# Performance work log

Measured on AMD Instinct MI355X. Metric: run time of the kernel, lower is better.

The kernel has to match this reference:

```python
import jax, jax.numpy as jnp
import numpy as np

B, N, M = 16, 2048, 2048


def setup_inputs() -> dict:
    key = jax.random.key(0)
    k1, k2, k3 = jax.random.split(key, 3)
    pred_dsmat = jax.random.uniform(k1, (B, N, M), dtype=jnp.float32)
    # valid sizes: src_ns <= tgt_ns so a permutation GT exists for every valid row
    src_ns = jax.random.randint(k2, (B,), 1024, 1537, dtype=jnp.int32)
    tgt_ns = jax.random.randint(k3, (B,), 1537, 2049, dtype=jnp.int32)
    # gt_perm: identity permutation restricted to the valid region (one 1 per valid row)
    i = jnp.arange(N)[:, None]
    j = jnp.arange(M)[None, :]
    eye = (i == j).astype(jnp.float32)  # [N, M]
    row_mask = (jnp.arange(N)[None, :] < src_ns[:, None]).astype(jnp.float32)  # [B, N]
    gt_perm = eye[None, :, :] * row_mask[:, :, None]  # [B, N, M]
    return {"pred_dsmat": pred_dsmat, "gt_perm": gt_perm,
            "src_ns": src_ns, "tgt_ns": tgt_ns, "beta_value": 0.1}


def reference(pred_dsmat, gt_perm, src_ns, tgt_ns, beta_value):
    Bn, Nn, Mn = pred_dsmat.shape
    row_mask = jnp.arange(Nn)[None, :] < src_ns[:, None]   # [B, N] bool
    col_mask = jnp.arange(Mn)[None, :] < tgt_ns[:, None]   # [B, M] bool
    mask = row_mask[:, :, None] & col_mask[:, None, :]     # [B, N, M]

    pred = jnp.clip(pred_dsmat, 0.0, 1.0) * mask
    gt = gt_perm * mask

    gt_pred = pred * gt                      # gt-selected predicted values
    row_gt = gt_pred.sum(axis=2)             # [B, N] per-row GT value
    col_gt = gt_pred.sum(axis=1)             # [B, M] per-col GT value
    row_cnt = gt.sum(axis=2)                 # [B, N] #GT matches per row
    col_cnt = gt.sum(axis=1)                 # [B, M] #GT matches per col

    # attention masks: entries >= (gt value - beta), restricted to valid region
    att_src = ((pred >= row_gt[:, :, None] - beta_value) & mask) * row_cnt[:, :, None]
    att_tgt = ((pred >= col_gt[:, None, :] - beta_value) & mask) * col_cnt[:, None, :]

    src_neg = jnp.sum(((att_src - gt) * pred) ** 2, axis=2)  # [B, N]
    src_pos = jnp.sum(gt_pred ** 2, axis=2)                  # [B, N]
    tgt_neg = jnp.sum(((att_tgt - gt) * pred) ** 2, axis=1)  # [B, M]

    # sum of tgt_neg over the GT-matched column of each row == dot with column counts
    corr = jnp.einsum('bm,bm->b', tgt_neg, col_cnt)          # [B]

    denom = 1.0 + src_neg + corr[:, None]                    # [B, N]
    num = jnp.where(row_mask, src_pos, 1.0)
    den = jnp.where(row_mask, denom, 1.0)
    loss = -0.5 * jnp.sum(jnp.log(num / den) * row_mask)
    n_sum = src_ns.sum().astype(pred.dtype)
    return loss / n_sum
```

## Files before the change

### kernel.cpp

```cpp
#include <hip/hip_runtime.h>

#define B_ 16
#define N_ 2048
#define M_ 2048
#define RROWS 8
#define WROWS 2
#define CHUNK 1024
#define NCHUNK (M_ / CHUNK)
#define JCH (CHUNK / 256)
#define DROWS 32
#define DWROWS 8
#define KCAP 4

__device__ __forceinline__ float wave_sum(float v) {
#pragma unroll
    for (int off = 32; off >= 1; off >>= 1) v += __shfl_xor(v, off);
    return v;
}

extern "C" __global__ __launch_bounds__(256) void k_gt(
    const float* __restrict__ gt, const float* __restrict__ pred,
    const int* __restrict__ src_ns, const int* __restrict__ tgt_ns,
    int* __restrict__ nnz, int* __restrict__ ent_col,
    float* __restrict__ ent_val,
    float* __restrict__ row_gt, float* __restrict__ row_cnt,
    float* __restrict__ colS_gt, float* __restrict__ colS_cnt,
    int* flag)
{
    const int b = blockIdx.y;
    const int src = src_ns[b];
    const int band = blockIdx.x;
    if (band * RROWS >= src) return;
    const int tgt = tgt_ns[b];
    const int c0 = blockIdx.z * CHUNK;
    if (tgt - c0 <= 0) return;
    const int wave = threadIdx.x >> 6, lane = threadIdx.x & 63;
    const int bfull = b * (N_ * M_);
    const int bc = bfull + c0;

    const int row0 = band * RROWS + wave * WROWS;
    for (int r = 0; r < WROWS; ++r) {
        const int n = row0 + r;
        if (n >= src) break;
        const int ri = b * N_ + n;
        const float4* grow = (const float4*)(gt + bc + n * M_);
        const float4 g0 = grow[lane];
        const float4 g1 = grow[64 + lane];
        const float4 g2 = grow[128 + lane];
        const float4 g3 = grow[192 + lane];
#define GTEST(GV, J) \
        if (GV.x != 0.f || GV.y != 0.f || GV.z != 0.f || GV.w != 0.f) { \
            const int mb = c0 + (J * 64 + lane) * 4; \
            GC(GV, 0, x); GC(GV, 1, y); GC(GV, 2, z); GC(GV, 3, w); \
        }
#define GC(GV, KK, MB) do { \
    const int c = mb + KK; \
    const float gv = GV.MB; \
    if (gv != 0.f && c < tgt) { \
        const int slot = atomicAdd(&nnz[ri], 1); \
        if (slot < KCAP) { \
            ent_col[ri * KCAP + slot] = c; ent_val[ri * KCAP + slot] = gv; \
            float pv = pred[bfull + n * M_ + c]; \
            pv = fminf(fmaxf(pv, 0.f), 1.f); \
            const float gp = gv * pv; \
            atomicAdd(&row_gt[ri], gp); \
            atomicAdd(&row_cnt[ri], gv); \
            atomicAdd(&colS_gt[b * M_ + c], gp); \
            atomicAdd(&colS_cnt[b * M_ + c], gv); \
        } else *flag = 1; \
    } \
} while (0)
        GTEST(g0, 0) GTEST(g1, 1) GTEST(g2, 2) GTEST(g3, 3)
#undef GC
#undef GTEST
    }
}

extern "C" __global__ __launch_bounds__(256) void k_p1d(
    const float* __restrict__ pred, const float* __restrict__ gt,
    const int* __restrict__ src_ns, const int* __restrict__ tgt_ns,
    const int* flag,
    float* __restrict__ row_gt, float* __restrict__ row_cnt,
    float* __restrict__ colD_gt, float* __restrict__ colD_cnt)
{
    if (*flag == 0) return;
    const int b = blockIdx.y;
    const int src = src_ns[b];
    const int band = blockIdx.x;
    if (band * DROWS >= src) return;
    const int tgt = tgt_ns[b];
    const int wave = threadIdx.x >> 6, lane = threadIdx.x & 63;
    const int base = b * (N_ * M_);

    float4 acg[8], accn[8];
#pragma unroll
    for (int j = 0; j < 8; ++j) { acg[j] = make_float4(0,0,0,0); accn[j] = make_float4(0,0,0,0); }

    const int row0 = band * DROWS + wave * DWROWS;
    for (int r = 0; r < DWROWS; ++r) {
        const int n = row0 + r;
        if (n >= src) break;
        const float4* prow = (const float4*)(pred + base + n * M_);
        const float4* grow = (const float4*)(gt + base + n * M_);
        float rg = 0.f, rc = 0.f;
#pragma unroll
        for (int j = 0; j < 8; ++j) {
            const int m4 = j * 64 + lane;
            const float4 p4 = prow[m4];
            const float4 g4 = grow[m4];
            const int mb = m4 * 4;
#define P1C(KK, MB) do { \
    const bool ok = (mb + KK) < tgt; \
    float p = fminf(fmaxf(p4.MB, 0.f), 1.f); p = ok ? p : 0.f; \
    const float g = ok ? g4.MB : 0.f; \
    const float gp = p * g; \
    rg += gp; rc += g; \
    acg[j].MB += gp; accn[j].MB += g; \
} while (0)
            P1C(0, x); P1C(1, y); P1C(2, z); P1C(3, w);
#undef P1C
        }
        rg = wave_sum(rg); rc = wave_sum(rc);
        if (lane == 0) { row_gt[b * N_ + n] = rg; row_cnt[b * N_ + n] = rc; }
    }

    __shared__ float4 s_cg[M_ / 4];
    __shared__ float4 s_cc[M_ / 4];
    for (int i = threadIdx.x; i < M_ / 4; i += 256) {
        s_cg[i] = make_float4(0,0,0,0);
        s_cc[i] = make_float4(0,0,0,0);
    }
    __syncthreads();
    for (int w = 0; w < 4; ++w) {
        if (wave == w) {
#pragma unroll
            for (int j = 0; j < 8; ++j) {
                const int i = j * 64 + lane;
                float4 v = s_cg[i];
                v.x += acg[j].x; v.y += acg[j].y; v.z += acg[j].z; v.w += acg[j].w;
                s_cg[i] = v;
                float4 u = s_cc[i];
                u.x += accn[j].x; u.y += accn[j].y; u.z += accn[j].z; u.w += accn[j].w;
                s_cc[i] = u;
            }
        }
        __syncthreads();
    }
    const float* fcg = (const float*)s_cg;
    const float* fcc = (const float*)s_cc;
    for (int i = threadIdx.x; i < M_; i += 256) {
        atomicAdd(&colD_gt[b * M_ + i], fcg[i]);
        atomicAdd(&colD_cnt[b * M_ + i], fcc[i]);
    }
}

extern "C" __global__ __launch_bounds__(256) void k_pred(
    const float* __restrict__ pred, const float* __restrict__ gt,
    const int* __restrict__ src_ns, const int* __restrict__ tgt_ns,
    const float* __restrict__ beta_p,
    const float* __restrict__ row_gt, const float* __restrict__ row_cnt,
    const float* __restrict__ colS_gt, const float* __restrict__ colS_cnt,
    const float* __restrict__ colD_gt, const float* __restrict__ colD_cnt,
    const int* __restrict__ nnz, const int* __restrict__ ent_col,
    const float* __restrict__ ent_val, const int* flag,
    float* __restrict__ src_neg, float* __restrict__ src_pos,
    float* __restrict__ corr)
{
    const int b = blockIdx.y;
    const int src = src_ns[b];
    const int band = blockIdx.x;
    if (band * RROWS >= src) return;
    const int tgt = tgt_ns[b];
    const int c0 = blockIdx.z * CHUNK;
    const bool chunk0 = (c0 == 0);
    if (tgt - c0 <= 0 && !chunk0) return;
    const float beta = beta_p[0];
    const int wave = threadIdx.x >> 6, lane = threadIdx.x & 63;
    const int bfull = b * (N_ * M_);
    const int bc = bfull + c0;
    const bool dense = (*flag != 0);
    const float* __restrict__ cgq = dense ? colD_gt : colS_gt;
    const float* __restrict__ ccq = dense ? colD_cnt : colS_cnt;

    float4 cgb[JCH], cc[JCH], tn[JCH];
    const float4* cg4 = (const float4*)(cgq + b * M_ + c0);
    const float4* cc4 = (const float4*)(ccq + b * M_ + c0);
#pragma unroll
    for (int j = 0; j < JCH; ++j) {
        float4 v = cg4[j * 64 + lane];
        v.x -= beta; v.y -= beta; v.z -= beta; v.w -= beta;
        cgb[j] = v;
        cc[j] = cc4[j * 64 + lane];
        tn[j] = make_float4(0,0,0,0);
    }

    float cadd = 0.f;
    const int row0 = band * RROWS + wave * WROWS;
    if (!dense) {
        for (int r = 0; r < WROWS; ++r) {
            const int n = row0 + r;
            if (n >= src) break;
            const int ri = b * N_ + n;
            const float rc = row_cnt[ri];
            const float rth = row_gt[ri] - beta;
            const float4* prow = (const float4*)(pred + bc + n * M_);
            const float4 p0 = prow[lane];
            const float4 p1 = prow[64 + lane];
            const float4 p2 = prow[128 + lane];
            const float4 p3 = prow[192 + lane];
            float sneg = 0.f;
#define P2S(PV, J, KK, MB) do { \
    const bool ok = (c0 + (J * 64 + lane) * 4 + KK) < tgt; \
    float p = fminf(fmaxf(PV.MB, 0.f), 1.f); p = ok ? p : 0.f; \
    const float as = (p >= rth) ? rc : 0.f; \
    const float ds = as * p; \
    sneg += ds * ds; \
    const float at = (p >= cgb[J].MB) ? cc[J].MB : 0.f; \
    const float d = at * p; \
    tn[J].MB += d * d; \
} while (0)
#define P2SV(PV, J) P2S(PV, J, 0, x); P2S(PV, J, 1, y); P2S(PV, J, 2, z); P2S(PV, J, 3, w);
            P2SV(p0, 0) P2SV(p1, 1) P2SV(p2, 2) P2SV(p3, 3)
#undef P2SV
#undef P2S
            sneg = wave_sum(sneg);
            if (lane == 0) {
                if (chunk0) {
                    float spos = 0.f;
                    const int nn0 = nnz[ri];
                    const int nn = nn0 < KCAP ? nn0 : KCAP;
                    for (int s = 0; s < nn; ++s) {
                        const int c = ent_col[ri * KCAP + s];
                        const float gv = ent_val[ri * KCAP + s];
                        float pv = pred[bfull + n * M_ + c];
                        pv = fminf(fmaxf(pv, 0.f), 1.f);
                        const float as = (pv >= rth) ? rc : 0.f;
                        const float d0 = as * pv;
                        const float d1 = (as - gv) * pv;
                        sneg += d1 * d1 - d0 * d0;
                        const float gp = gv * pv;
                        spos += gp * gp;
                        const float ccv = ccq[b * M_ + c];
                        const float at = (pv >= cgq[b * M_ + c] - beta) ? ccv : 0.f;
                        const float t0 = at * pv;
                        const float t1 = (at - gv) * pv;
                        cadd += (t1 * t1 - t0 * t0) * ccv;
                    }
                    atomicAdd(&src_pos[ri], spos);
                }
                atomicAdd(&src_neg[ri], sneg);
            }
        }
    } else {
        for (int r = 0; r < WROWS; ++r) {
            const int n = row0 + r;
            if (n >= src) break;
            const int ri = b * N_ + n;
            const float rc = row_cnt[ri];
            const float rth = row_gt[ri] - beta;
            const float4* prow = (const float4*)(pred + bc + n * M_);
            const float4* grow = (const float4*)(gt + bc + n * M_);
            const float4 p0 = prow[lane];
            const float4 p1 = prow[64 + lane];
            const float4 p2 = prow[128 + lane];
            const float4 p3 = prow[192 + lane];
            const float4 g0 = grow[lane];
            const float4 g1 = grow[64 + lane];
            const float4 g2 = grow[128 + lane];
            const float4 g3 = grow[192 + lane];
            float sneg = 0.f, spos = 0.f;
#define P2D(PV, GV, J, KK, MB) do { \
    const bool ok = (c0 + (J * 64 + lane) * 4 + KK) < tgt; \
    float p = fminf(fmaxf(PV.MB, 0.f), 1.f); p = ok ? p : 0.f; \
    const float gv = ok ? GV.MB : 0.f; \
    const float as = (p >= rth) ? rc : 0.f; \
    const float ds = (as - gv) * p; \
    sneg += ds * ds; \
    const float gp = gv * p; spos += gp * gp; \
    const float at = (p >= cgb[J].MB) ? cc[J].MB : 0.f; \
    const float dt = (at - gv) * p; \
    tn[J].MB += dt * dt; \
} while (0)
#define P2DV(PV, GV, J) P2D(PV, GV, J, 0, x); P2D(PV, GV, J, 1, y); P2D(PV, GV, J, 2, z); P2D(PV, GV, J, 3, w);
            P2DV(p0, g0, 0) P2DV(p1, g1, 1) P2DV(p2, g2, 2) P2DV(p3, g3, 3)
#undef P2DV
#undef P2D
            sneg = wave_sum(sneg); spos = wave_sum(spos);
            if (lane == 0) {
                atomicAdd(&src_neg[ri], sneg);
                atomicAdd(&src_pos[ri], spos);
            }
        }
    }

    float dp = cadd;
#pragma unroll
    for (int j = 0; j < JCH; ++j)
        dp += tn[j].x * cc[j].x + tn[j].y * cc[j].y + tn[j].z * cc[j].z + tn[j].w * cc[j].w;
    dp = wave_sum(dp);
    __shared__ float sred[4];
    if (lane == 0) sred[wave] = dp;
    __syncthreads();
    if (threadIdx.x == 0)
        atomicAdd(&corr[b], sred[0] + sred[1] + sred[2] + sred[3]);
}

extern "C" __global__ __launch_bounds__(256) void k_final(
    const float* __restrict__ src_neg, const float* __restrict__ src_pos,
    const float* __restrict__ corr_p, const int* __restrict__ src_ns,
    float* __restrict__ out)
{
    const int b = blockIdx.x >> 3;
    const int part = blockIdx.x & 7;
    const int wave = threadIdx.x >> 6, lane = threadIdx.x & 63;
    const int src = src_ns[b];
    const int n0 = part * (N_ / 8);
    const float corr = corr_p[b];

    float ls = 0.f;
    const int n = n0 + threadIdx.x;
    if (n < src) {
        const float sp = src_pos[b * N_ + n];
        const float sn = src_neg[b * N_ + n];
        ls = logf(sp) - logf(1.f + sn + corr);
    }
    ls = wave_sum(ls);
    __shared__ float sredl[4];
    if (lane == 0) sredl[wave] = ls;
    __syncthreads();
    if (threadIdx.x == 0) {
        const float total = sredl[0] + sredl[1] + sredl[2] + sredl[3];
        if (total != 0.f) {
            float nsum = 0.f;
            for (int i = 0; i < B_; ++i) nsum += (float)src_ns[i];
            atomicAdd(out, -0.5f * total / nsum);
        }
    }
}

extern "C" void kernel_launch(void* const* d_in, const int* in_sizes, int n_in,
                              void* d_out, int out_size, void* d_ws, size_t ws_size,
                              hipStream_t stream)
{
    const float* pred   = (const float*)d_in[0];
    const float* gtp    = (const float*)d_in[1];
    const int*   src_ns = (const int*)d_in[2];
    const int*   tgt_ns = (const int*)d_in[3];
    const float* beta   = (const float*)d_in[4];
    float* out = (float*)d_out;
    float* ws  = (float*)d_ws;

    float* colS_gt  = ws;
    float* colS_cnt = colS_gt  + B_ * M_;
    float* colD_gt  = colS_cnt + B_ * M_;
    float* colD_cnt = colD_gt  + B_ * M_;
    float* row_gt   = colD_cnt + B_ * M_;
    float* row_cnt  = row_gt   + B_ * N_;
    float* src_neg  = row_cnt  + B_ * N_;
    float* src_pos  = src_neg  + B_ * N_;
    float* corr     = src_pos  + B_ * N_;
    int*   nnz      = (int*)(corr + B_);
    int*   flag     = nnz + B_ * N_;
    int*   ent_col  = (int*)(flag + 1);
    float* ent_val  = (float*)(ent_col + B_ * N_ * KCAP);

    const size_t zero_bytes = (size_t)(4 * B_ * M_ + 5 * B_ * N_ + B_ + 1) * sizeof(float);
    hipMemsetAsync(d_ws, 0, zero_bytes, stream);
    hipMemsetAsync(d_out, 0, sizeof(float), stream);

    dim3 gsplit(N_ / RROWS, B_, NCHUNK);
    k_gt<<<gsplit, 256, 0, stream>>>(gtp, pred, src_ns, tgt_ns,
                                     nnz, ent_col, ent_val,
                                     row_gt, row_cnt, colS_gt, colS_cnt, flag);
    k_p1d<<<dim3(N_ / DROWS, B_), 256, 0, stream>>>(pred, gtp, src_ns, tgt_ns, flag,
                                                    row_gt, row_cnt, colD_gt, colD_cnt);
    k_pred<<<gsplit, 256, 0, stream>>>(pred, gtp, src_ns, tgt_ns, beta,
                                       row_gt, row_cnt,
                                       colS_gt, colS_cnt, colD_gt, colD_cnt,
                                       nnz, ent_col, ent_val, flag,
                                       src_neg, src_pos, corr);
    k_final<<<B_ * 8, 256, 0, stream>>>(src_neg, src_pos, corr, src_ns, out);
}
```

Baseline: 515.9 us.

## Prefetch next row in gt and sparse loss kernels, double rows per wave, precompute column masks

Doubles the rows handled per block and per wave (RROWS 16, WROWS 4). The k_gt scan and the sparse path of the loss kernel now software-pipeline their row loads, issuing the next row's float4 loads before processing the current row. The per-element column bound check is replaced by float masks computed once per chunk and applied by multiplication. Together these aim to hide memory latency and cut per-element ALU work, at the cost of more registers and half as many blocks.

```diff
diff --git a/kernel.cpp b/kernel.cpp
--- a/kernel.cpp
+++ b/kernel.cpp
@@ -3,8 +3,8 @@
 #define B_ 16
 #define N_ 2048
 #define M_ 2048
-#define RROWS 8
-#define WROWS 2
+#define RROWS 16
+#define WROWS 4
 #define CHUNK 1024
 #define NCHUNK (M_ / CHUNK)
 #define JCH (CHUNK / 256)
@@ -39,15 +39,26 @@
     const int bc = bfull + c0;
 
     const int row0 = band * RROWS + wave * WROWS;
-    for (int r = 0; r < WROWS; ++r) {
+    int rmax = src - row0; if (rmax > WROWS) rmax = WROWS;
+    if (rmax <= 0) return;
+
+    const float* gbase = gt + bc + row0 * M_;
+    const float4* grow = (const float4*)gbase;
+    float4 a0 = grow[lane];
+    float4 a1 = grow[64 + lane];
+    float4 a2 = grow[128 + lane];
+    float4 a3 = grow[192 + lane];
+    for (int r = 0; r < rmax; ++r) {
+        float4 b0, b1, b2, b3;
+        if (r + 1 < rmax) {
+            const float4* nrow = (const float4*)(gbase + (r + 1) * M_);
+            b0 = nrow[lane]; b1 = nrow[64 + lane];
+            b2 = nrow[128 + lane]; b3 = nrow[192 + lane];
+        } else {
+            b0 = b1 = b2 = b3 = make_float4(0,0,0,0);
+        }
         const int n = row0 + r;
-        if (n >= src) break;
         const int ri = b * N_ + n;
-        const float4* grow = (const float4*)(gt + bc + n * M_);
-        const float4 g0 = grow[lane];
-        const float4 g1 = grow[64 + lane];
-        const float4 g2 = grow[128 + lane];
-        const float4 g3 = grow[192 + lane];
 #define GTEST(GV, J) \
         if (GV.x != 0.f || GV.y != 0.f || GV.z != 0.f || GV.w != 0.f) { \
             const int mb = c0 + (J * 64 + lane) * 4; \
@@ -70,9 +81,10 @@
         } else *flag = 1; \
     } \
 } while (0)
-        GTEST(g0, 0) GTEST(g1, 1) GTEST(g2, 2) GTEST(g3, 3)
+        GTEST(a0, 0) GTEST(a1, 1) GTEST(a2, 2) GTEST(a3, 3)
 #undef GC
 #undef GTEST
+        a0 = b0; a1 = b1; a2 = b2; a3 = b3;
     }
 }
 
@@ -182,7 +194,7 @@
     const float* __restrict__ cgq = dense ? colD_gt : colS_gt;
     const float* __restrict__ ccq = dense ? colD_cnt : colS_cnt;
 
-    float4 cgb[JCH], cc[JCH], tn[JCH];
+    float4 cgb[JCH], cc[JCH], tn[JCH], msk[JCH];
     const float4* cg4 = (const float4*)(cgq + b * M_ + c0);
     const float4* cc4 = (const float4*)(ccq + b * M_ + c0);
 #pragma unroll
@@ -192,26 +204,41 @@
         cgb[j] = v;
         cc[j] = cc4[j * 64 + lane];
         tn[j] = make_float4(0,0,0,0);
+        const int mb = c0 + (j * 64 + lane) * 4;
+        msk[j].x = (mb + 0 < tgt) ? 1.f : 0.f;
+        msk[j].y = (mb + 1 < tgt) ? 1.f : 0.f;
+        msk[j].z = (mb + 2 < tgt) ? 1.f : 0.f;
+        msk[j].w = (mb + 3 < tgt) ? 1.f : 0.f;
     }
 
     float cadd = 0.f;
     const int row0 = band * RROWS + wave * WROWS;
+    int rmax = src - row0; if (rmax > WROWS) rmax = WROWS;
+
     if (!dense) {
-        for (int r = 0; r < WROWS; ++r) {
-            const int n = row0 + r;
-            if (n >= src) break;
-            const int ri = b * N_ + n;
-            const float rc = row_cnt[ri];
-            const float rth = row_gt[ri] - beta;
-            const float4* prow = (const float4*)(pred + bc + n * M_);
-            const float4 p0 = prow[lane];
-            const float4 p1 = prow[64 + lane];
-            const float4 p2 = prow[128 + lane];
-            const float4 p3 = prow[192 + lane];
-            float sneg = 0.f;
-#define P2S(PV, J, KK, MB) do { \
-    const bool ok = (c0 + (J * 64 + lane) * 4 + KK) < tgt; \
-    float p = fminf(fmaxf(PV.MB, 0.f), 1.f); p = ok ? p : 0.f; \
+        if (rmax > 0) {
+            const float* pbase = pred + bc + row0 * M_;
+            const float4* prow = (const float4*)pbase;
+            float4 a0 = prow[lane];
+            float4 a1 = prow[64 + lane];
+            float4 a2 = prow[128 + lane];
+            float4 a3 = prow[192 + lane];
+            for (int r = 0; r < rmax; ++r) {
+                float4 q0, q1, q2, q3;
+                if (r + 1 < rmax) {
+                    const float4* nrow = (const float4*)(pbase + (r + 1) * M_);
+                    q0 = nrow[lane]; q1 = nrow[64 + lane];
+                    q2 = nrow[128 + lane]; q3 = nrow[192 + lane];
+                } else {
+                    q0 = q1 = q2 = q3 = make_float4(0,0,0,0);
+                }
+                const int n = row0 + r;
+                const int ri = b * N_ + n;
+                const float rc = row_cnt[ri];
+                const float rth = row_gt[ri] - beta;
+                float sneg = 0.f;
+#define P2S(PV, J, MB) do { \
+    const float p = fminf(fmaxf(PV.MB, 0.f), 1.f) * msk[J].MB; \
     const float as = (p >= rth) ? rc : 0.f; \
     const float ds = as * p; \
     sneg += ds * ds; \
@@ -219,42 +246,43 @@
     const float d = at * p; \
     tn[J].MB += d * d; \
 } while (0)
-#define P2SV(PV, J) P2S(PV, J, 0, x); P2S(PV, J, 1, y); P2S(PV, J, 2, z); P2S(PV, J, 3, w);
-            P2SV(p0, 0) P2SV(p1, 1) P2SV(p2, 2) P2SV(p3, 3)
+#define P2SV(PV, J) P2S(PV, J, x); P2S(PV, J, y); P2S(PV, J, z); P2S(PV, J, w);
+                P2SV(a0, 0) P2SV(a1, 1) P2SV(a2, 2) P2SV(a3, 3)
 #undef P2SV
 #undef P2S
-            sneg = wave_sum(sneg);
-            if (lane == 0) {
-                if (chunk0) {
-                    float spos = 0.f;
-                    const int nn0 = nnz[ri];
-                    const int nn = nn0 < KCAP ? nn0 : KCAP;
-                    for (int s = 0; s < nn; ++s) {
-                        const int c = ent_col[ri * KCAP + s];
-                        const float gv = ent_val[ri * KCAP + s];
-                        float pv = pred[bfull + n * M_ + c];
-                        pv = fminf(fmaxf(pv, 0.f), 1.f);
-                        const float as = (pv >= rth) ? rc : 0.f;
-                        const float d0 = as * pv;
-                        const float d1 = (as - gv) * pv;
-                        sneg += d1 * d1 - d0 * d0;
-                        const float gp = gv * pv;
-                        spos += gp * gp;
-                        const float ccv = ccq[b * M_ + c];
-                        const float at = (pv >= cgq[b * M_ + c] - beta) ? ccv : 0.f;
-                        const float t0 = at * pv;
-                        const float t1 = (at - gv) * pv;
-                        cadd += (t1 * t1 - t0 * t0) * ccv;
+                sneg = wave_sum(sneg);
+                if (lane == 0) {
+                    if (chunk0) {
+                        float spos = 0.f;
+                        const int nn0 = nnz[ri];
+                        const int nn = nn0 < KCAP ? nn0 : KCAP;
+                        for (int s = 0; s < nn; ++s) {
+                            const int c = ent_col[ri * KCAP + s];
+                            const float gv = ent_val[ri * KCAP + s];
+                            float pv = pred[bfull + n * M_ + c];
+                            pv = fminf(fmaxf(pv, 0.f), 1.f);
+                            const float as = (pv >= rth) ? rc : 0.f;
+                            const float d0 = as * pv;
+                            const float d1 = (as - gv) * pv;
+                            sneg += d1 * d1 - d0 * d0;
+                            const float gp = gv * pv;
+                            spos += gp * gp;
+                            const float ccv = ccq[b * M_ + c];
+                            const float at = (pv >= cgq[b * M_ + c] - beta) ? ccv : 0.f;
+                            const float t0 = at * pv;
+                            const float t1 = (at - gv) * pv;
+                            cadd += (t1 * t1 - t0 * t0) * ccv;
+                        }
+                        atomicAdd(&src_pos[ri], spos);
                     }
-                    atomicAdd(&src_pos[ri], spos);
+                    atomicAdd(&src_neg[ri], sneg);
                 }
-                atomicAdd(&src_neg[ri], sneg);
+                a0 = q0; a1 = q1; a2 = q2; a3 = q3;
             }
         }
     } else {
-        for (int r = 0; r < WROWS; ++r) {
+        for (int r = 0; r < rmax; ++r) {
             const int n = row0 + r;
-            if (n >= src) break;
             const int ri = b * N_ + n;
             const float rc = row_cnt[ri];
             const float rth = row_gt[ri] - beta;
@@ -269,10 +297,9 @@
             const float4 g2 = grow[128 + lane];
             const float4 g3 = grow[192 + lane];
             float sneg = 0.f, spos = 0.f;
-#define P2D(PV, GV, J, KK, MB) do { \
-    const bool ok = (c0 + (J * 64 + lane) * 4 + KK) < tgt; \
-    float p = fminf(fmaxf(PV.MB, 0.f), 1.f); p = ok ? p : 0.f; \
-    const float gv = ok ? GV.MB : 0.f; \
+#define P2D(PV, GV, J, MB) do { \
+    const float p = fminf(fmaxf(PV.MB, 0.f), 1.f) * msk[J].MB; \
+    const float gv = GV.MB * msk[J].MB; \
     const float as = (p >= rth) ? rc : 0.f; \
     const float ds = (as - gv) * p; \
     sneg += ds * ds; \
@@ -281,7 +308,7 @@
     const float dt = (at - gv) * p; \
     tn[J].MB += dt * dt; \
 } while (0)
-#define P2DV(PV, GV, J) P2D(PV, GV, J, 0, x); P2D(PV, GV, J, 1, y); P2D(PV, GV, J, 2, z); P2D(PV, GV, J, 3, w);
+#define P2DV(PV, GV, J) P2D(PV, GV, J, x); P2D(PV, GV, J, y); P2D(PV, GV, J, z); P2D(PV, GV, J, w);
             P2DV(p0, g0, 0) P2DV(p1, g1, 1) P2DV(p2, g2, 2) P2DV(p3, g3, 3)
 #undef P2DV
 #undef P2D
```

Result: faster. 500.2 us (-3.0%).
